# Performance work log

Measured on AMD Instinct MI355X. Metric: run time of the kernel, lower is better.

The kernel has to match this reference:

```python
import jax, jax.numpy as jnp
import numpy as np

# Dimensions inferred from the module (few-shot reweighted YOLOv2 region loss)
B, C, NA, NCPA = 64, 20, 5, 1          # batch, base classes, anchors, classes-per-anchor
H, W = 19, 19                           # feature map (608 input / stride 32)
T = 50                                  # cfg.max_boxes
THRESH = 0.6
COORD_SCALE = 1.0
CLASS_SCALE = 1.0
NB = B * C                              # per-class 'image' rows, as in the torch code
A4 = NA * H * W
EPS = 1e-12
BCE_EPS = 1e-7
ANCHORS = [[1.3221, 1.73145], [3.19275, 4.00944], [5.05587, 8.09892], [9.47112, 4.84053], [11.2364, 10.0071]]


def iou_xywh(x1, y1, w1, h1, x2, y2, w2, h2):
    # center-size IoU, matches darknet bbox_iou(x1y1x2y2=False)
    l = jnp.maximum(x1 - w1 * 0.5, x2 - w2 * 0.5)
    r = jnp.minimum(x1 + w1 * 0.5, x2 + w2 * 0.5)
    t = jnp.maximum(y1 - h1 * 0.5, y2 - h2 * 0.5)
    b = jnp.minimum(y1 + h1 * 0.5, y2 + h2 * 0.5)
    inter = jnp.clip(r - l, 0.0) * jnp.clip(b - t, 0.0)
    union = w1 * h1 + w2 * h2 - inter
    return inter / jnp.maximum(union, EPS)


def setup_inputs() -> dict:
    key = jax.random.key(0)
    k1, k2, k3, k4 = jax.random.split(key, 4)
    output = jax.random.normal(k1, (NB, NA * (5 + NCPA), H, W), jnp.float32) * 0.5
    # target rows: [cls, x, y, w, h] * T, coords in (0,1); x kept > 0 so all boxes are 'valid'
    cls_ids = jax.random.randint(k2, (B, C, T), 0, C).astype(jnp.float32)
    xy = jax.random.uniform(k3, (B, C, T, 2), minval=0.05, maxval=0.95)
    wh = jax.random.uniform(k4, (B, C, T, 2), minval=0.05, maxval=0.5)
    target = jnp.concatenate([cls_ids[..., None], xy, wh], axis=-1).reshape(B, C, T * 5)
    anchors = jnp.asarray(ANCHORS, jnp.float32)
    return {"output": output, "target": target, "anchors": anchors}


def _forward(output, target, anchors):
    target = jax.lax.stop_gradient(target)
    anchors = jax.lax.stop_gradient(anchors)
    out5 = output.reshape(NB, NA, 5 + NCPA, H, W)
    x = jax.nn.sigmoid(out5[:, :, 0])
    y = jax.nn.sigmoid(out5[:, :, 1])
    w = out5[:, :, 2]
    h = out5[:, :, 3]
    conf = jax.nn.sigmoid(out5[:, :, 4])
    # class logits regrouped to original batch: (B*NA*H*W, C)
    cls = out5[:, :, 5:5 + NCPA].reshape(NB, NA, H, W)
    cls_logits = cls.reshape(B, C, NA * H * W).transpose(0, 2, 1).reshape(-1, C)
    # decode pred boxes (detached, mirroring torch's use of .data)
    grid_x = jnp.arange(W, dtype=jnp.float32)[None, None, None, :]
    grid_y = jnp.arange(H, dtype=jnp.float32)[None, None, :, None]
    aw = anchors[:, 0][None, :, None, None]
    ah = anchors[:, 1][None, :, None, None]
    px = jax.lax.stop_gradient(x) + grid_x
    py = jax.lax.stop_gradient(y) + grid_y
    pw = jnp.exp(jax.lax.stop_gradient(w)) * aw
    ph = jnp.exp(jax.lax.stop_gradient(h)) * ah
    # ground-truth boxes per row
    tgt = target.reshape(NB, T, 5)
    cls_t = tgt[:, :, 0]
    gx = tgt[:, :, 1] * W
    gy = tgt[:, :, 2] * H
    gw = tgt[:, :, 3] * W
    gh = tgt[:, :, 4] * H
    # 'break on first zero x' semantics
    valid = jnp.cumprod((tgt[:, :, 1] != 0).astype(jnp.int32), axis=1) > 0
    # stage 1: zero conf_mask where any gt IoU > thresh (scan over T to avoid (NB,T,A4) blowup)
    pxf = px.reshape(NB, A4); pyf = py.reshape(NB, A4)
    pwf = pw.reshape(NB, A4); phf = ph.reshape(NB, A4)

    def iou_step(ci, xs):
        gxt, gyt, gwt, ght, vt = xs
        iou = iou_xywh(pxf, pyf, pwf, phf, gxt[:, None], gyt[:, None], gwt[:, None], ght[:, None])
        return jnp.maximum(ci, jnp.where(vt[:, None], iou, 0.0)), None

    cur_ious, _ = jax.lax.scan(iou_step, jnp.zeros((NB, A4), jnp.float32), (gx.T, gy.T, gw.T, gh.T, valid.T))
    conf_mask0 = jnp.where(cur_ious.reshape(NB, NA, H, W) > THRESH, 0.0, 1.0)
    # best anchor per gt by wh-only IoU
    inter = jnp.minimum(gw[..., None], anchors[:, 0]) * jnp.minimum(gh[..., None], anchors[:, 1])
    union = gw[..., None] * gh[..., None] + anchors[:, 0] * anchors[:, 1] - inter
    best_n = jnp.argmax(inter / jnp.maximum(union, EPS), axis=-1).astype(jnp.int32)  # (NB,T)
    gi = gx.astype(jnp.int32)
    gj = gy.astype(jnp.int32)
    # stage 2: ordered scatter of targets (later boxes overwrite earlier, as in the torch loops)
    binds = jnp.arange(NB)
    z = jnp.zeros((NB, NA, H, W), jnp.float32)
    # seen < 12800 branch: tx=ty=0.5, tw=th=0, coord_mask=1
    carry0 = (jnp.ones_like(z), z, conf_mask0, jnp.full_like(z, 0.5), jnp.full_like(z, 0.5), z, z, z, z)

    def tgt_step(carry, xs):
        cm, clm, cfm, tx, ty, tw, th, tconf, tcls = carry
        gxt, gyt, gwt, ght, bn, git, gjt, vt, ct = xs
        idx = (binds, bn, gjt, git)

        def upd(arr, val):
            return arr.at[idx].set(jnp.where(vt, val, arr[idx]))

        aw_b = anchors[bn, 0]
        ah_b = anchors[bn, 1]
        iou = iou_xywh(gxt, gyt, gwt, ght, px[idx], py[idx], pw[idx], ph[idx])
        cm = upd(cm, 1.0)
        clm = upd(clm, 1.0)
        cfm = upd(cfm, 1.0)
        tx = upd(tx, gxt - git.astype(jnp.float32))
        ty = upd(ty, gyt - gjt.astype(jnp.float32))
        tw = upd(tw, jnp.log(jnp.maximum(gwt, EPS) / aw_b))
        th = upd(th, jnp.log(jnp.maximum(ght, EPS) / ah_b))
        tconf = upd(tconf, iou)
        tcls = upd(tcls, ct)
        return (cm, clm, cfm, tx, ty, tw, th, tconf, tcls), None

    xs = (gx.T, gy.T, gw.T, gh.T, best_n.T, gi.T, gj.T, valid.T, cls_t.T)
    (coord_mask, cls_mask, conf_mask, tx, ty, tw, th, tconf, tcls), _ = jax.lax.scan(tgt_step, carry0, xs)
    # regroup per-class rows back to original batch (neg_ratio='full' -> counts[i] == C)
    cm_grp = cls_mask.reshape(B, C, NA, H, W).sum(axis=1)
    tcls_grp = tcls.reshape(B, C, NA, H, W).sum(axis=1)
    sel = (cm_grp == 1.0).reshape(-1)           # exclude colliding cells
    labels = tcls_grp.reshape(-1).astype(jnp.int32)

    def bce_mean(p, t):
        p = jnp.clip(p, BCE_EPS, 1.0 - BCE_EPS)
        return jnp.mean(-(t * jnp.log(p) + (1.0 - t) * jnp.log(1.0 - p)))

    loss_x = COORD_SCALE * bce_mean(x * coord_mask, tx * coord_mask)
    loss_y = COORD_SCALE * bce_mean(y * coord_mask, ty * coord_mask)
    loss_w = COORD_SCALE * 0.5 * jnp.mean((w * coord_mask - tw * coord_mask) ** 2)
    loss_h = COORD_SCALE * 0.5 * jnp.mean((h * coord_mask - th * coord_mask) ** 2)
    loss_conf = 0.5 * jnp.mean((conf * conf_mask - tconf * conf_mask) ** 2)
    logp = jax.nn.log_softmax(cls_logits, axis=-1)
    nll = -jnp.take_along_axis(logp, labels[:, None], axis=1)[:, 0]
    nsel = jnp.maximum(jnp.sum(sel.astype(jnp.float32)), 1.0)
    loss_cls = CLASS_SCALE * jnp.sum(jnp.where(sel, nll, 0.0)) / nsel
    return loss_x + loss_y + loss_w + loss_h + loss_conf + loss_cls


def reference(output, target, anchors):
    return _forward(output, target, anchors)
```

## Files before the change

kernel.cpp:

```cpp
#include <hip/hip_runtime.h>
#include <math.h>

constexpr int cB   = 64;
constexpr int cC   = 20;
constexpr int cNA  = 5;
constexpr int cH   = 19;
constexpr int cW   = 19;
constexpr int cT   = 50;
constexpr int cNB  = cB * cC;
constexpr int cHW  = cH * cW;
constexpr int cA4  = cNA * cHW;
constexpr int cCH  = cNA * 6;
constexpr long cNTOT = (long)cNB * cA4;
constexpr int cCLS_ROWS = cB * cA4;

constexpr int ACC_BANKS = 64;
constexpr int TGT_N   = cNB * cT;
constexpr size_t OFF_GX  = 4096;
constexpr size_t OFF_GY  = OFF_GX  + (size_t)TGT_N * 4;
constexpr size_t OFF_GW  = OFF_GY  + (size_t)TGT_N * 4;
constexpr size_t OFF_GH  = OFF_GW  + (size_t)TGT_N * 4;
constexpr size_t OFF_CLS = OFF_GH  + (size_t)TGT_N * 4;
constexpr size_t OFF_VAL = OFF_CLS + (size_t)TGT_N * 4;
constexpr size_t OFF_WIN = OFF_VAL + (size_t)TGT_N * 4;

__device__ __forceinline__ float fexp(float x) {
    return __builtin_amdgcn_exp2f(x * 1.4426950408889634f);
}
__device__ __forceinline__ float flog(float x) {
    return __builtin_amdgcn_logf(x) * 0.6931471805599453f;
}
__device__ __forceinline__ float frcp(float x) { return __builtin_amdgcn_rcpf(x); }
__device__ __forceinline__ float fsigmoid(float x) { return frcp(1.0f + fexp(-x)); }

__global__ void k_prep(const float* __restrict__ target, const float* __restrict__ anch,
                       float* __restrict__ gx_, float* __restrict__ gy_,
                       float* __restrict__ gw_, float* __restrict__ gh_,
                       float* __restrict__ cls_, int* __restrict__ val_,
                       int* __restrict__ winner, double* __restrict__ acc) {
    const int nb = blockIdx.x;
    const int t  = threadIdx.x;
    if (nb == 0) {
        for (int k = t; k < 5 * ACC_BANKS; k += 64) acc[k] = 0.0;
    }
    float cv = 0.f, xr = 1.f, yr = 0.f, wr = 0.f, hr = 0.f;
    if (t < cT) {
        const float* tg = target + (size_t)nb * (cT * 5) + t * 5;
        cv = tg[0]; xr = tg[1]; yr = tg[2]; wr = tg[3]; hr = tg[4];
    }
    unsigned long long nz = __ballot(xr != 0.0f);
    bool valid = false;
    if (t < cT) {
        unsigned long long below = (t == 63) ? ~0ull : ((2ull << t) - 1ull);
        valid = ((~nz) & below) == 0ull;
        float gx = xr * (float)cW, gy = yr * (float)cH;
        float gw = wr * (float)cW, gh = hr * (float)cH;
        int o = nb * cT + t;
        gx_[o] = gx; gy_[o] = gy; gw_[o] = gw; gh_[o] = gh;
        cls_[o] = cv; val_[o] = valid ? 1 : 0;
        float best = -1.0f; int bn = 0;
        for (int n = 0; n < cNA; ++n) {
            float aw = anch[2*n], ah = anch[2*n+1];
            float inter = fminf(gw, aw) * fminf(gh, ah);
            float uni   = gw*gh + aw*ah - inter;
            float r = inter / fmaxf(uni, 1e-12f);
            if (r > best) { best = r; bn = n; }
        }
        if (valid) {
            int gi = (int)gx, gj = (int)gy;
            atomicMax(&winner[(size_t)nb * cA4 + bn * cHW + gj * cW + gi], t);
        }
    }
}

__launch_bounds__(256)
__global__ void k_main(const float* __restrict__ outp, const float* __restrict__ anch,
                       const float* __restrict__ gx_, const float* __restrict__ gy_,
                       const float* __restrict__ gw_, const float* __restrict__ gh_,
                       const int* __restrict__ val_, const int* __restrict__ winner,
                       double* __restrict__ acc) {
    __shared__ float4 s_box[cT];
    __shared__ float  s_ga06[cT];
    __shared__ float  s_gx[cT], s_gy[cT], s_gw[cT], s_gh[cT];
    __shared__ float  s_aw[cNA], s_ah[cNA];
    __shared__ double s_red[3][4];
    const int tid  = threadIdx.x;
    const int nb   = blockIdx.x >> 1;
    const int base = ((blockIdx.x & 1) << 10) + tid;

    if (tid < cT) {
        int o = nb * cT + tid;
        float gx = gx_[o], gy = gy_[o], gw = gw_[o], gh = gh_[o];
        s_gx[tid] = gx; s_gy[tid] = gy; s_gw[tid] = gw; s_gh[tid] = gh;
        if (val_[o]) {
            s_box[tid]  = make_float4(gx - 0.5f*gw, gx + 0.5f*gw, gy - 0.5f*gh, gy + 0.5f*gh);
            s_ga06[tid] = 0.6f * (gw * gh);
        } else {
            s_box[tid]  = make_float4(1e30f, -1e30f, 1e30f, -1e30f);
            s_ga06[tid] = 0.0f;
        }
    }
    if (tid < cNA) { s_aw[tid] = anch[2*tid]; s_ah[tid] = anch[2*tid+1]; }
    __syncthreads();

    float pl[4], pr[4], pt[4], pb[4], pa06[4], ov[4];
    float conf[4], tconf[4];
    bool  wflag[4], active[4];
    float bce = 0.0f, sq = 0.0f;

    #pragma unroll
    for (int u = 0; u < 4; ++u) {
        int cell = base + (u << 8);
        bool act = cell < cA4;
        active[u] = act; wflag[u] = false;
        conf[u] = 0.0f; tconf[u] = 0.0f; ov[u] = -1e30f;
        if (act) {
            int na  = cell / cHW;
            int rem = cell - na * cHW;
            int j   = rem / cW;
            int i   = rem - j * cW;
            const float* ob = outp + (size_t)nb * (cCH * cHW) + (size_t)(na * 6) * cHW + rem;
            float xl = ob[0], yl = ob[cHW], wl = ob[2*cHW], hl = ob[3*cHW], cl = ob[4*cHW];
            float x  = fsigmoid(xl);
            float y  = fsigmoid(yl);
            float cf = fsigmoid(cl);
            float px = x + (float)i, py = y + (float)j;
            float pw = fexp(wl) * s_aw[na], ph = fexp(hl) * s_ah[na];
            float l0 = px - 0.5f*pw, r0 = px + 0.5f*pw;
            float t0 = py - 0.5f*ph, b0 = py + 0.5f*ph;
            float pa = pw * ph;
            pl[u] = l0; pr[u] = r0; pt[u] = t0; pb[u] = b0;
            pa06[u] = 0.6f * pa;
            conf[u] = cf;
            float tx = 0.5f, ty = 0.5f, tw = 0.0f, th = 0.0f;
            int wt = winner[(size_t)nb * cA4 + cell];
            if (wt >= 0) {
                wflag[u] = true;
                float gx = s_gx[wt], gy = s_gy[wt], gw = s_gw[wt], gh = s_gh[wt];
                tx = gx - (float)i; ty = gy - (float)j;
                tw = flog(fmaxf(gw, 1e-12f) * frcp(s_aw[na]));
                th = flog(fmaxf(gh, 1e-12f) * frcp(s_ah[na]));
                float iw = fminf(r0, gx + 0.5f*gw) - fmaxf(l0, gx - 0.5f*gw);
                float ih = fminf(b0, gy + 0.5f*gh) - fmaxf(t0, gy - 0.5f*gh);
                iw = fmaxf(iw, 0.0f); ih = fmaxf(ih, 0.0f);
                float inter = iw * ih;
                float uni   = gw*gh + pa - inter;
                tconf[u] = inter * frcp(fmaxf(uni, 1e-12f));
            }
            float pc = fminf(fmaxf(x, 1e-7f), 1.0f - 1e-7f);
            bce += -(tx * flog(pc) + (1.0f - tx) * flog(1.0f - pc));
            pc = fminf(fmaxf(y, 1e-7f), 1.0f - 1e-7f);
            bce += -(ty * flog(pc) + (1.0f - ty) * flog(1.0f - pc));
            float dw = wl - tw, dh = hl - th;
            sq += dw*dw + dh*dh;
        } else {
            pl[u] = 1e30f; pr[u] = -1e30f; pt[u] = 1e30f; pb[u] = -1e30f; pa06[u] = 0.0f;
        }
    }

    for (int t = 0; t < cT; ++t) {
        float4 bx = s_box[t];
        float  ga = s_ga06[t];
        #pragma unroll
        for (int u = 0; u < 4; ++u) {
            float iw = fminf(pr[u], bx.y) - fmaxf(pl[u], bx.x);
            float ih = fminf(pb[u], bx.w) - fmaxf(pt[u], bx.z);
            iw = fmaxf(iw, 0.0f); ih = fmaxf(ih, 0.0f);
            float inter = iw * ih;
            ov[u] = fmaxf(ov[u], __builtin_fmaf(1.6f, inter, -ga));
        }
    }

    float sc = 0.0f;
    #pragma unroll
    for (int u = 0; u < 4; ++u) {
        if (!active[u]) continue;
        bool over = ov[u] > pa06[u];
        float cm = wflag[u] ? 1.0f : (over ? 0.0f : 1.0f);
        float d  = (conf[u] - tconf[u]) * cm;
        sc += d * d;
    }

    double v0 = (double)bce, v1 = (double)sq, v2 = (double)sc;
    for (int off = 32; off > 0; off >>= 1) {
        v0 += __shfl_down(v0, off);
        v1 += __shfl_down(v1, off);
        v2 += __shfl_down(v2, off);
    }
    int lane = tid & 63, wid = tid >> 6;
    if (lane == 0) { s_red[0][wid] = v0; s_red[1][wid] = v1; s_red[2][wid] = v2; }
    __syncthreads();
    if (tid == 0) {
        double a0 = s_red[0][0] + s_red[0][1] + s_red[0][2] + s_red[0][3];
        double a1 = s_red[1][0] + s_red[1][1] + s_red[1][2] + s_red[1][3];
        double a2 = s_red[2][0] + s_red[2][1] + s_red[2][2] + s_red[2][3];
        int bank = blockIdx.x & (ACC_BANKS - 1);
        atomicAdd(&acc[0*ACC_BANKS + bank], a0);
        atomicAdd(&acc[1*ACC_BANKS + bank], a1);
        atomicAdd(&acc[2*ACC_BANKS + bank], a2);
    }
}

__launch_bounds__(256)
__global__ void k_cls(const float* __restrict__ outp, const float* __restrict__ cls_,
                      const int* __restrict__ winner, double* __restrict__ acc) {
    __shared__ double s_red[2][4];
    int tid = threadIdx.x;
    int row = blockIdx.x * 256 + tid;
    double nll = 0.0, ns = 0.0;
    if (row < cCLS_ROWS) {
        int b = row / cA4;
        int a = row - b * cA4;
        int cnt = 0, selc = -1, selw = -1;
        for (int c = 0; c < cC; ++c) {
            int wv = winner[(size_t)(b * cC + c) * cA4 + a];
            if (wv >= 0) { cnt++; selc = c; selw = wv; }
        }
        if (cnt == 1) {
            int na  = a / cHW;
            int rem = a - na * cHW;
            const float* ob = outp + ((size_t)b * cC * cCH + na * 6 + 5) * cHW + rem;
            float l[cC]; float m = -1e30f;
            for (int c = 0; c < cC; ++c) { l[c] = ob[(size_t)c * cCH * cHW]; m = fmaxf(m, l[c]); }
            float s = 0.0f;
            for (int c = 0; c < cC; ++c) s += fexp(l[c] - m);
            int label = (int)cls_[(b * cC + selc) * cT + selw];
            nll = (double)(m + flog(s) - l[label]);
            ns  = 1.0;
        }
    }
    for (int off = 32; off > 0; off >>= 1) {
        nll += __shfl_down(nll, off);
        ns  += __shfl_down(ns, off);
    }
    int lane = tid & 63, wid = tid >> 6;
    if (lane == 0) { s_red[0][wid] = nll; s_red[1][wid] = ns; }
    __syncthreads();
    if (tid == 0) {
        double a0 = s_red[0][0] + s_red[0][1] + s_red[0][2] + s_red[0][3];
        double a1 = s_red[1][0] + s_red[1][1] + s_red[1][2] + s_red[1][3];
        int bank = blockIdx.x & (ACC_BANKS - 1);
        atomicAdd(&acc[3*ACC_BANKS + bank], a0);
        atomicAdd(&acc[4*ACC_BANKS + bank], a1);
    }
}

__global__ void k_final(const double* __restrict__ acc, float* __restrict__ o) {
    int lane = threadIdx.x;
    double s[5];
    #pragma unroll
    for (int j = 0; j < 5; ++j) {
        double v = acc[j * ACC_BANKS + lane];
        for (int off = 32; off > 0; off >>= 1) v += __shfl_down(v, off);
        s[j] = v;
    }
    if (lane == 0) {
        double Ninv = 1.0 / (double)cNTOT;
        double loss = s[0] * Ninv
                    + 0.5 * s[1] * Ninv
                    + 0.5 * s[2] * Ninv
                    + s[3] / fmax(s[4], 1.0);
        o[0] = (float)loss;
    }
}

extern "C" void kernel_launch(void* const* d_in, const int* in_sizes, int n_in,
                              void* d_out, int out_size, void* d_ws, size_t ws_size,
                              hipStream_t stream) {
    const float* output = (const float*)d_in[0];
    const float* target = (const float*)d_in[1];
    const float* anch   = (const float*)d_in[2];
    char* ws = (char*)d_ws;
    double* acc  = (double*)ws;
    float* gx_   = (float*)(ws + OFF_GX);
    float* gy_   = (float*)(ws + OFF_GY);
    float* gw_   = (float*)(ws + OFF_GW);
    float* gh_   = (float*)(ws + OFF_GH);
    float* cls_  = (float*)(ws + OFF_CLS);
    int*   val_  = (int*)  (ws + OFF_VAL);
    int*   winner= (int*)  (ws + OFF_WIN);

    hipMemsetAsync(winner, 0xFF, (size_t)cNTOT * 4, stream);

    k_prep<<<cNB, 64, 0, stream>>>(target, anch, gx_, gy_, gw_, gh_, cls_, val_, winner, acc);
    k_main<<<cNB * 2, 256, 0, stream>>>(output, anch, gx_, gy_, gw_, gh_, val_, winner, acc);
    k_cls<<<(cCLS_ROWS + 255) / 256, 256, 0, stream>>>(output, cls_, winner, acc);
    k_final<<<1, 64, 0, stream>>>(acc, (float*)d_out);
}
```

Measured before the change: 145.5 us.

## Precompute GT boxes in prep and process whole image per block in k_main

Moves the GT box edge and area-threshold computation into k_prep, which writes them to workspace arrays, and drops the shared-memory staging and syncthreads from k_main. k_main now uses one block per image with 8 cells per thread instead of two blocks with 4 cells each, reading the box data directly from global/scalar memory. To limit register pressure it recomputes the sigmoids and reloads the outputs in a second pass, and it also unrolls the loops in k_cls. The tradeoff is fewer blocks, more registers per thread, and redundant loads and transcendental work, in exchange for amortising the per-box setup across more cells.

After: 145.9 us. About the same (+0.3%).

```diff
diff --git a/kernel.cpp b/kernel.cpp
--- a/kernel.cpp
+++ b/kernel.cpp
@@ -16,13 +16,18 @@
 
 constexpr int ACC_BANKS = 64;
 constexpr int TGT_N   = cNB * cT;
+constexpr size_t SZT   = (size_t)TGT_N * 4;
 constexpr size_t OFF_GX  = 4096;
-constexpr size_t OFF_GY  = OFF_GX  + (size_t)TGT_N * 4;
-constexpr size_t OFF_GW  = OFF_GY  + (size_t)TGT_N * 4;
-constexpr size_t OFF_GH  = OFF_GW  + (size_t)TGT_N * 4;
-constexpr size_t OFF_CLS = OFF_GH  + (size_t)TGT_N * 4;
-constexpr size_t OFF_VAL = OFF_CLS + (size_t)TGT_N * 4;
-constexpr size_t OFF_WIN = OFF_VAL + (size_t)TGT_N * 4;
+constexpr size_t OFF_GY  = OFF_GX  + SZT;
+constexpr size_t OFF_GW  = OFF_GY  + SZT;
+constexpr size_t OFF_GH  = OFF_GW  + SZT;
+constexpr size_t OFF_CLS = OFF_GH  + SZT;
+constexpr size_t OFF_BL  = OFF_CLS + SZT;
+constexpr size_t OFF_BR  = OFF_BL  + SZT;
+constexpr size_t OFF_BT  = OFF_BR  + SZT;
+constexpr size_t OFF_BB  = OFF_BT  + SZT;
+constexpr size_t OFF_BGA = OFF_BB  + SZT;
+constexpr size_t OFF_WIN = OFF_BGA + SZT;
 
 __device__ __forceinline__ float fexp(float x) {
     return __builtin_amdgcn_exp2f(x * 1.4426950408889634f);
@@ -36,7 +41,10 @@
 __global__ void k_prep(const float* __restrict__ target, const float* __restrict__ anch,
                        float* __restrict__ gx_, float* __restrict__ gy_,
                        float* __restrict__ gw_, float* __restrict__ gh_,
-                       float* __restrict__ cls_, int* __restrict__ val_,
+                       float* __restrict__ cls_,
+                       float* __restrict__ bl_, float* __restrict__ br_,
+                       float* __restrict__ bt_, float* __restrict__ bb_,
+                       float* __restrict__ bga_,
                        int* __restrict__ winner, double* __restrict__ acc) {
     const int nb = blockIdx.x;
     const int t  = threadIdx.x;
@@ -49,15 +57,23 @@
         cv = tg[0]; xr = tg[1]; yr = tg[2]; wr = tg[3]; hr = tg[4];
     }
     unsigned long long nz = __ballot(xr != 0.0f);
-    bool valid = false;
     if (t < cT) {
         unsigned long long below = (t == 63) ? ~0ull : ((2ull << t) - 1ull);
-        valid = ((~nz) & below) == 0ull;
+        bool valid = ((~nz) & below) == 0ull;
         float gx = xr * (float)cW, gy = yr * (float)cH;
         float gw = wr * (float)cW, gh = hr * (float)cH;
         int o = nb * cT + t;
         gx_[o] = gx; gy_[o] = gy; gw_[o] = gw; gh_[o] = gh;
-        cls_[o] = cv; val_[o] = valid ? 1 : 0;
+        cls_[o] = cv;
+        if (valid) {
+            bl_[o] = gx - 0.5f * gw;  br_[o] = gx + 0.5f * gw;
+            bt_[o] = gy - 0.5f * gh;  bb_[o] = gy + 0.5f * gh;
+            bga_[o] = 0.6f * (gw * gh);
+        } else {
+            bl_[o] = 1e30f; br_[o] = -1e30f;
+            bt_[o] = 1e30f; bb_[o] = -1e30f;
+            bga_[o] = 0.0f;
+        }
         float best = -1.0f; int bn = 0;
         for (int n = 0; n < cNA; ++n) {
             float aw = anch[2*n], ah = anch[2*n+1];
@@ -77,108 +93,93 @@
 __global__ void k_main(const float* __restrict__ outp, const float* __restrict__ anch,
                        const float* __restrict__ gx_, const float* __restrict__ gy_,
                        const float* __restrict__ gw_, const float* __restrict__ gh_,
-                       const int* __restrict__ val_, const int* __restrict__ winner,
-                       double* __restrict__ acc) {
-    __shared__ float4 s_box[cT];
-    __shared__ float  s_ga06[cT];
-    __shared__ float  s_gx[cT], s_gy[cT], s_gw[cT], s_gh[cT];
-    __shared__ float  s_aw[cNA], s_ah[cNA];
+                       const float* __restrict__ bl_, const float* __restrict__ br_,
+                       const float* __restrict__ bt_, const float* __restrict__ bb_,
+                       const float* __restrict__ bga_,
+                       const int* __restrict__ winner, double* __restrict__ acc) {
     __shared__ double s_red[3][4];
-    const int tid  = threadIdx.x;
-    const int nb   = blockIdx.x >> 1;
-    const int base = ((blockIdx.x & 1) << 10) + tid;
-
-    if (tid < cT) {
-        int o = nb * cT + tid;
-        float gx = gx_[o], gy = gy_[o], gw = gw_[o], gh = gh_[o];
-        s_gx[tid] = gx; s_gy[tid] = gy; s_gw[tid] = gw; s_gh[tid] = gh;
-        if (val_[o]) {
-            s_box[tid]  = make_float4(gx - 0.5f*gw, gx + 0.5f*gw, gy - 0.5f*gh, gy + 0.5f*gh);
-            s_ga06[tid] = 0.6f * (gw * gh);
-        } else {
-            s_box[tid]  = make_float4(1e30f, -1e30f, 1e30f, -1e30f);
-            s_ga06[tid] = 0.0f;
-        }
-    }
-    if (tid < cNA) { s_aw[tid] = anch[2*tid]; s_ah[tid] = anch[2*tid+1]; }
-    __syncthreads();
-
-    float pl[4], pr[4], pt[4], pb[4], pa06[4], ov[4];
-    float conf[4], tconf[4];
-    bool  wflag[4], active[4];
-    float bce = 0.0f, sq = 0.0f;
+    const int tid = threadIdx.x;
+    const int nb  = blockIdx.x;
+    const int tb  = nb * cT;
+    const float* obase = outp + (size_t)nb * (cCH * cHW);
+
+    float pl[8], pr[8], pt[8], pb[8], pa06[8], ov[8];
 
     #pragma unroll
-    for (int u = 0; u < 4; ++u) {
-        int cell = base + (u << 8);
-        bool act = cell < cA4;
-        active[u] = act; wflag[u] = false;
-        conf[u] = 0.0f; tconf[u] = 0.0f; ov[u] = -1e30f;
-        if (act) {
-            int na  = cell / cHW;
-            int rem = cell - na * cHW;
-            int j   = rem / cW;
-            int i   = rem - j * cW;
-            const float* ob = outp + (size_t)nb * (cCH * cHW) + (size_t)(na * 6) * cHW + rem;
-            float xl = ob[0], yl = ob[cHW], wl = ob[2*cHW], hl = ob[3*cHW], cl = ob[4*cHW];
-            float x  = fsigmoid(xl);
-            float y  = fsigmoid(yl);
-            float cf = fsigmoid(cl);
-            float px = x + (float)i, py = y + (float)j;
-            float pw = fexp(wl) * s_aw[na], ph = fexp(hl) * s_ah[na];
-            float l0 = px - 0.5f*pw, r0 = px + 0.5f*pw;
-            float t0 = py - 0.5f*ph, b0 = py + 0.5f*ph;
-            float pa = pw * ph;
-            pl[u] = l0; pr[u] = r0; pt[u] = t0; pb[u] = b0;
-            pa06[u] = 0.6f * pa;
-            conf[u] = cf;
-            float tx = 0.5f, ty = 0.5f, tw = 0.0f, th = 0.0f;
-            int wt = winner[(size_t)nb * cA4 + cell];
-            if (wt >= 0) {
-                wflag[u] = true;
-                float gx = s_gx[wt], gy = s_gy[wt], gw = s_gw[wt], gh = s_gh[wt];
-                tx = gx - (float)i; ty = gy - (float)j;
-                tw = flog(fmaxf(gw, 1e-12f) * frcp(s_aw[na]));
-                th = flog(fmaxf(gh, 1e-12f) * frcp(s_ah[na]));
-                float iw = fminf(r0, gx + 0.5f*gw) - fmaxf(l0, gx - 0.5f*gw);
-                float ih = fminf(b0, gy + 0.5f*gh) - fmaxf(t0, gy - 0.5f*gh);
-                iw = fmaxf(iw, 0.0f); ih = fmaxf(ih, 0.0f);
-                float inter = iw * ih;
-                float uni   = gw*gh + pa - inter;
-                tconf[u] = inter * frcp(fmaxf(uni, 1e-12f));
-            }
+    for (int u = 0; u < 8; ++u) {
+        int cell = tid + (u << 8);
+        int cc   = (cell < cA4) ? cell : (cA4 - 1);
+        int na   = cc / cHW;
+        int rem  = cc - na * cHW;
+        int j    = rem / cW;
+        int i    = rem - j * cW;
+        const float* ob = obase + (size_t)(na * 6) * cHW + rem;
+        float xl = ob[0], yl = ob[cHW], wl = ob[2*cHW], hl = ob[3*cHW];
+        float aw = anch[2*na], ah = anch[2*na+1];
+        float x  = fsigmoid(xl), y = fsigmoid(yl);
+        float px = x + (float)i, py = y + (float)j;
+        float pw = fexp(wl) * aw, ph = fexp(hl) * ah;
+        pl[u] = px - 0.5f*pw; pr[u] = px + 0.5f*pw;
+        pt[u] = py - 0.5f*ph; pb[u] = py + 0.5f*ph;
+        pa06[u] = 0.6f * (pw * ph);
+        ov[u] = -1e30f;
+    }
+
+    #pragma unroll 5
+    for (int t = 0; t < cT; ++t) {
+        float sl = bl_[tb + t], sr = br_[tb + t];
+        float st = bt_[tb + t], sb = bb_[tb + t];
+        float sg = bga_[tb + t];
+        #pragma unroll
+        for (int u = 0; u < 8; ++u) {
+            float iw = fminf(pr[u], sr) - fmaxf(pl[u], sl);
+            float ih = fminf(pb[u], sb) - fmaxf(pt[u], st);
+            iw = fmaxf(iw, 0.0f); ih = fmaxf(ih, 0.0f);
+            ov[u] = fmaxf(ov[u], __builtin_fmaf(1.6f, iw * ih, -sg));
+        }
+    }
+
+    float bce = 0.0f, sq = 0.0f, sc = 0.0f;
+    #pragma unroll
+    for (int u = 0; u < 8; ++u) {
+        int cell = tid + (u << 8);
+        bool a_  = cell < cA4;
+        int cc   = a_ ? cell : (cA4 - 1);
+        int na   = cc / cHW;
+        int rem  = cc - na * cHW;
+        int j    = rem / cW;
+        int i    = rem - j * cW;
+        const float* ob = obase + (size_t)(na * 6) * cHW + rem;
+        float xl = ob[0], yl = ob[cHW], wl = ob[2*cHW], hl = ob[3*cHW], cl = ob[4*cHW];
+        float aw = anch[2*na], ah = anch[2*na+1];
+        float x  = fsigmoid(xl), y = fsigmoid(yl), cf = fsigmoid(cl);
+        float tx = 0.5f, ty = 0.5f, tw = 0.0f, th = 0.0f, tcf = 0.0f;
+        int wt = winner[(size_t)nb * cA4 + cc];
+        bool wfl = (wt >= 0) && a_;
+        if (wfl) {
+            float gx = gx_[tb+wt], gy = gy_[tb+wt], gw = gw_[tb+wt], gh = gh_[tb+wt];
+            tx = gx - (float)i; ty = gy - (float)j;
+            tw = flog(fmaxf(gw, 1e-12f) * frcp(aw));
+            th = flog(fmaxf(gh, 1e-12f) * frcp(ah));
+            float iw = fminf(pr[u], gx + 0.5f*gw) - fmaxf(pl[u], gx - 0.5f*gw);
+            float ih = fminf(pb[u], gy + 0.5f*gh) - fmaxf(pt[u], gy - 0.5f*gh);
+            iw = fmaxf(iw, 0.0f); ih = fmaxf(ih, 0.0f);
+            float inter = iw * ih;
+            float pa  = pa06[u] * (1.0f / 0.6f);
+            float uni = gw*gh + pa - inter;
+            tcf = inter * frcp(fmaxf(uni, 1e-12f));
+        }
+        if (a_) {
             float pc = fminf(fmaxf(x, 1e-7f), 1.0f - 1e-7f);
             bce += -(tx * flog(pc) + (1.0f - tx) * flog(1.0f - pc));
             pc = fminf(fmaxf(y, 1e-7f), 1.0f - 1e-7f);
             bce += -(ty * flog(pc) + (1.0f - ty) * flog(1.0f - pc));
             float dw = wl - tw, dh = hl - th;
             sq += dw*dw + dh*dh;
-        } else {
-            pl[u] = 1e30f; pr[u] = -1e30f; pt[u] = 1e30f; pb[u] = -1e30f; pa06[u] = 0.0f;
-        }
-    }
-
-    for (int t = 0; t < cT; ++t) {
-        float4 bx = s_box[t];
-        float  ga = s_ga06[t];
-        #pragma unroll
-        for (int u = 0; u < 4; ++u) {
-            float iw = fminf(pr[u], bx.y) - fmaxf(pl[u], bx.x);
-            float ih = fminf(pb[u], bx.w) - fmaxf(pt[u], bx.z);
-            iw = fmaxf(iw, 0.0f); ih = fmaxf(ih, 0.0f);
-            float inter = iw * ih;
-            ov[u] = fmaxf(ov[u], __builtin_fmaf(1.6f, inter, -ga));
-        }
-    }
-
-    float sc = 0.0f;
-    #pragma unroll
-    for (int u = 0; u < 4; ++u) {
-        if (!active[u]) continue;
-        bool over = ov[u] > pa06[u];
-        float cm = wflag[u] ? 1.0f : (over ? 0.0f : 1.0f);
-        float d  = (conf[u] - tconf[u]) * cm;
-        sc += d * d;
+            float cm = wfl ? 1.0f : ((ov[u] > pa06[u]) ? 0.0f : 1.0f);
+            float d  = (cf - tcf) * cm;
+            sc += d * d;
+        }
     }
 
     double v0 = (double)bce, v1 = (double)sq, v2 = (double)sc;
@@ -194,7 +195,7 @@
         double a0 = s_red[0][0] + s_red[0][1] + s_red[0][2] + s_red[0][3];
         double a1 = s_red[1][0] + s_red[1][1] + s_red[1][2] + s_red[1][3];
         double a2 = s_red[2][0] + s_red[2][1] + s_red[2][2] + s_red[2][3];
-        int bank = blockIdx.x & (ACC_BANKS - 1);
+        int bank = nb & (ACC_BANKS - 1);
         atomicAdd(&acc[0*ACC_BANKS + bank], a0);
         atomicAdd(&acc[1*ACC_BANKS + bank], a1);
         atomicAdd(&acc[2*ACC_BANKS + bank], a2);
@@ -212,6 +213,7 @@
         int b = row / cA4;
         int a = row - b * cA4;
         int cnt = 0, selc = -1, selw = -1;
+        #pragma unroll
         for (int c = 0; c < cC; ++c) {
             int wv = winner[(size_t)(b * cC + c) * cA4 + a];
             if (wv >= 0) { cnt++; selc = c; selw = wv; }
@@ -221,8 +223,10 @@
             int rem = a - na * cHW;
             const float* ob = outp + ((size_t)b * cC * cCH + na * 6 + 5) * cHW + rem;
             float l[cC]; float m = -1e30f;
+            #pragma unroll
             for (int c = 0; c < cC; ++c) { l[c] = ob[(size_t)c * cCH * cHW]; m = fmaxf(m, l[c]); }
             float s = 0.0f;
+            #pragma unroll
             for (int c = 0; c < cC; ++c) s += fexp(l[c] - m);
             int label = (int)cls_[(b * cC + selc) * cT + selw];
             nll = (double)(m + flog(s) - l[label]);
@@ -277,13 +281,19 @@
     float* gw_   = (float*)(ws + OFF_GW);
     float* gh_   = (float*)(ws + OFF_GH);
     float* cls_  = (float*)(ws + OFF_CLS);
-    int*   val_  = (int*)  (ws + OFF_VAL);
+    float* bl_   = (float*)(ws + OFF_BL);
+    float* br_   = (float*)(ws + OFF_BR);
+    float* bt_   = (float*)(ws + OFF_BT);
+    float* bb_   = (float*)(ws + OFF_BB);
+    float* bga_  = (float*)(ws + OFF_BGA);
     int*   winner= (int*)  (ws + OFF_WIN);
 
     hipMemsetAsync(winner, 0xFF, (size_t)cNTOT * 4, stream);
 
-    k_prep<<<cNB, 64, 0, stream>>>(target, anch, gx_, gy_, gw_, gh_, cls_, val_, winner, acc);
-    k_main<<<cNB * 2, 256, 0, stream>>>(output, anch, gx_, gy_, gw_, gh_, val_, winner, acc);
+    k_prep<<<cNB, 64, 0, stream>>>(target, anch, gx_, gy_, gw_, gh_, cls_,
+                                   bl_, br_, bt_, bb_, bga_, winner, acc);
+    k_main<<<cNB, 256, 0, stream>>>(output, anch, gx_, gy_, gw_, gh_,
+                                    bl_, br_, bt_, bb_, bga_, winner, acc);
     k_cls<<<(cCLS_ROWS + 255) / 256, 256, 0, stream>>>(output, cls_, winner, acc);
     k_final<<<1, 64, 0, stream>>>(acc, (float*)d_out);
 }
```
